# Optimization experiments

Hardware: AMD Instinct MI355X
Metric: run time of the kernel (lower is better)

Reference implementation:

```python
import jax, jax.numpy as jnp
import numpy as np

FEATURE_DIM = 1024
HIDDEN_DIM = FEATURE_DIM // 4  # MetaNet default: max(input_dim//4, output_dim) = 256
NUM_TASKS = 8
BATCH = 8192


def setup_inputs() -> dict:
    key = jax.random.key(0)
    ks = jax.random.split(key, 8)
    features = jax.random.normal(ks[0], (BATCH, FEATURE_DIM), dtype=jnp.float32)
    # meta_net: Linear(D->H) -> ReLU -> Linear(H->K). Scaled so coefficients straddle the threshold.
    W1 = jax.random.normal(ks[1], (HIDDEN_DIM, FEATURE_DIM), dtype=jnp.float32) * 0.02
    b1 = jax.random.normal(ks[2], (HIDDEN_DIM,), dtype=jnp.float32) * 0.01
    W2 = jax.random.normal(ks[3], (NUM_TASKS, HIDDEN_DIM), dtype=jnp.float32) * 0.1
    b2 = jax.random.normal(ks[4], (NUM_TASKS,), dtype=jnp.float32) * 0.05
    # per-task feature transforms, init randn * 0.01 as in the module
    task_mats = jax.random.normal(ks[5], (NUM_TASKS, FEATURE_DIM, FEATURE_DIM), dtype=jnp.float32) * 0.01
    # projection initialized to identity (nn.init.eye_)
    proj_W = jnp.eye(FEATURE_DIM, dtype=jnp.float32)
    base_threshold = jnp.array([0.05], dtype=jnp.float32)
    beta = jnp.array([1.0], dtype=jnp.float32)
    return {"features": features, "W1": W1, "b1": b1, "W2": W2, "b2": b2,
            "task_mats": task_mats, "proj_W": proj_W,
            "base_threshold": base_threshold, "beta": beta}


def reference(features, W1, b1, W2, b2, task_mats, proj_W, base_threshold, beta):
    # --- meta_net forward: coefficients [B, K] ---
    h = features @ W1.T + b1                    # [B, H]
    relu_h = jnp.maximum(h, 0.0)
    coeffs = relu_h @ W2.T + b2                 # [B, K]

    # --- gradient-based uncertainty: ||d coeff_k / d features_b||_2 ---
    # Jacobian of the 2-layer MLP: J[b,k,d] = sum_h W2[k,h] * relu'(h[b,h]) * W1[h,d]
    mask = (h > 0).astype(features.dtype)       # [B, H]
    J = jnp.einsum('kh,bh,hd->bkd', W2, mask, W1)   # [B, K, D]
    unc = jnp.sqrt(jnp.sum(J * J, axis=-1))     # [B, K]
    mx = jnp.max(unc)
    unc = jnp.where(mx > 0, unc / mx, unc)
    # torch computes this on detached features with create_graph=False -> non-differentiable
    unc = jax.lax.stop_gradient(unc)

    # --- adaptive gating ---
    base = jax.nn.softplus(base_threshold)                  # [1]
    thresholds = base * (1.0 + jax.nn.relu(beta) * unc)     # [B, K]
    gated = jnp.where(jnp.abs(coeffs) < thresholds, 0.0, coeffs)  # [B, K]

    # --- sequential weighted task-vector combination (blockwise=False) ---
    x = features                                # [B, D]
    for j in range(task_mats.shape[0]):         # small fixed K, structurally sequential
        x = x + gated[:, j:j + 1] * (x @ task_mats[j])
    return x @ proj_W.T                         # [B, D]
```

## Files before the change

### kernel.cpp

```cpp
#include <hip/hip_runtime.h>


typedef float  f32x4  __attribute__((ext_vector_type(4)));
typedef __bf16 bf16x8 __attribute__((ext_vector_type(8)));
typedef _Float16 f16x8 __attribute__((ext_vector_type(8)));
typedef _Float16 f16x4 __attribute__((ext_vector_type(4)));

__device__ __forceinline__ unsigned short f2bf(float x) {
  return __builtin_bit_cast(unsigned short, (__bf16)x);
}
__device__ __forceinline__ float bf2f(unsigned short u) {
  return (float)__builtin_bit_cast(__bf16, u);
}
__device__ __forceinline__ void ldsload16(void* lds, const void* g) {
  __builtin_amdgcn_global_load_lds(
      (const __attribute__((address_space(1))) void*)g,
      (__attribute__((address_space(3))) void*)lds, 16, 0, 0);
}


__global__ __launch_bounds__(256) void k_initsplit(const float* __restrict__ F,
                                                   _Float16* __restrict__ hi,
                                                   _Float16* __restrict__ lo,
                                                   float* __restrict__ xout,
                                                   unsigned short* __restrict__ xhA,
                                                   unsigned short* __restrict__ xhB) {
  size_t i = (size_t)blockIdx.x * 256 + threadIdx.x;
  float4 f = *(const float4*)&F[i * 4];
  _Float16 h0 = (_Float16)f.x, h1 = (_Float16)f.y, h2 = (_Float16)f.z, h3 = (_Float16)f.w;
  *(f16x4*)&hi[i * 4] = (f16x4){h0, h1, h2, h3};
  *(f16x4*)&lo[i * 4] = (f16x4){(_Float16)((f.x - (float)h0) * 2048.0f),
                                (_Float16)((f.y - (float)h1) * 2048.0f),
                                (_Float16)((f.z - (float)h2) * 2048.0f),
                                (_Float16)((f.w - (float)h3) * 2048.0f)};
  *(float4*)&xout[i * 4] = f;
  ushort4 u;
  u.x = f2bf(f.x); u.y = f2bf(f.y); u.z = f2bf(f.z); u.w = f2bf(f.w);
  *(ushort4*)&xhA[i * 4] = u;
  *(ushort4*)&xhB[i * 4] = u;
}

__global__ __launch_bounds__(256) void k_split(const float* __restrict__ src,
                                               _Float16* __restrict__ hi,
                                               _Float16* __restrict__ lo) {
  size_t i = (size_t)blockIdx.x * 256 + threadIdx.x;
  float4 f = *(const float4*)&src[i * 4];
  _Float16 h0 = (_Float16)f.x, h1 = (_Float16)f.y, h2 = (_Float16)f.z, h3 = (_Float16)f.w;
  *(f16x4*)&hi[i * 4] = (f16x4){h0, h1, h2, h3};
  *(f16x4*)&lo[i * 4] = (f16x4){(_Float16)((f.x - (float)h0) * 2048.0f),
                                (_Float16)((f.y - (float)h1) * 2048.0f),
                                (_Float16)((f.z - (float)h2) * 2048.0f),
                                (_Float16)((f.w - (float)h3) * 2048.0f)};
}

__global__ __launch_bounds__(256) void k_gram(const float* __restrict__ W1,
                                              float* __restrict__ G) {
  __shared__ float Wa[16][33], Wb[16][33];
  int t = threadIdx.x, ti = t & 15, tj = t >> 4;
  int bi = blockIdx.x, bj = blockIdx.y;
  float acc = 0.f;
  for (int kc = 0; kc < 1024; kc += 32) {
    __syncthreads();
    for (int e = t; e < 512; e += 256) {
      int r = e >> 5, k = e & 31;
      Wa[r][k] = W1[(size_t)(bi * 16 + r) * 1024 + kc + k];
      Wb[r][k] = W1[(size_t)(bj * 16 + r) * 1024 + kc + k];
    }
    __syncthreads();
#pragma unroll
    for (int k = 0; k < 32; k++) acc += Wa[ti][k] * Wb[tj][k];
  }
  G[(size_t)(bi * 16 + ti) * 256 + bj * 16 + tj] = acc;
}

__global__ __launch_bounds__(256) void k_prepA(const float* __restrict__ W2,
                                               const float* __restrict__ G,
                                               unsigned short* __restrict__ Bk,
                                               unsigned int* __restrict__ mx,
                                               int* __restrict__ cnt,
                                               int* __restrict__ cnt2,
                                               unsigned int* __restrict__ flag) {
  int k = blockIdx.x >> 8, hr = blockIdx.x & 255, t = threadIdx.x;
  if (blockIdx.x == 0) {
    if (t == 0) { *mx = 0u; *flag = 1u; }
    if (t < 8) { cnt[t] = 0; cnt2[t] = 0; }
  }
  float v = W2[k * 256 + hr] * W2[k * 256 + t] * G[(size_t)hr * 256 + t];
  float hi = bf2f(f2bf(v));
  float lo = v - hi;
  unsigned short* row = &Bk[((size_t)k * 256 + hr) * 512];
  row[t] = f2bf(hi);
  row[256 + t] = f2bf(lo);
}

__global__ __launch_bounds__(256) void k_maskcoef(const float* __restrict__ h,
                                                  const float* __restrict__ W2,
                                                  const float* __restrict__ b2,
                                                  unsigned short* __restrict__ Mb,
                                                  unsigned int* __restrict__ Mbits,
                                                  float* __restrict__ coeffs) {
  __shared__ float W2s[2048];
  __shared__ unsigned sw[4][8];
  int t = threadIdx.x;
  for (int e = t; e < 2048; e += 256) W2s[e] = W2[e];
  int w = t >> 6, l = t & 63;
  int row = blockIdx.x * 4 + w;
  float4 hv = *(const float4*)&h[(size_t)row * 256 + l * 4];
  ushort4 mv;
  mv.x = hv.x > 0.f ? 0x3F80 : 0; mv.y = hv.y > 0.f ? 0x3F80 : 0;
  mv.z = hv.z > 0.f ? 0x3F80 : 0; mv.w = hv.w > 0.f ? 0x3F80 : 0;
  *(ushort4*)&Mb[(size_t)row * 256 + l * 4] = mv;
  unsigned nib = (hv.x > 0.f ? 1u : 0u) | (hv.y > 0.f ? 2u : 0u) |
                 (hv.z > 0.f ? 4u : 0u) | (hv.w > 0.f ? 8u : 0u);
  if (l < 8) sw[w][l] = 0u;
  __syncthreads();
  atomicOr(&sw[w][l >> 3], nib << ((l & 7) * 4));
  __syncthreads();
  if (l < 8) Mbits[row * 8 + l] = sw[w][l];
  float r0 = fmaxf(hv.x, 0.f), r1 = fmaxf(hv.y, 0.f);
  float r2 = fmaxf(hv.z, 0.f), r3 = fmaxf(hv.w, 0.f);
#pragma unroll
  for (int k = 0; k < 8; k++) {
    const float* wr = &W2s[k * 256 + l * 4];
    float p = r0 * wr[0] + r1 * wr[1] + r2 * wr[2] + r3 * wr[3];
    p += __shfl_xor(p, 1);  p += __shfl_xor(p, 2);  p += __shfl_xor(p, 4);
    p += __shfl_xor(p, 8);  p += __shfl_xor(p, 16); p += __shfl_xor(p, 32);
    if (l == 0) coeffs[row * 8 + k] = p + b2[k];
  }
}

__global__ __launch_bounds__(256) void k_max(const float* __restrict__ unc2,
                                             unsigned int* __restrict__ mx) {
  int i = blockIdx.x * 256 + threadIdx.x;
  float v = 0.f;
  for (; i < 65536; i += 64 * 256) v = fmaxf(v, unc2[i]);
#pragma unroll
  for (int d = 1; d < 64; d <<= 1) v = fmaxf(v, __shfl_xor(v, d));
  __shared__ float sm[4];
  if ((threadIdx.x & 63) == 0) sm[threadIdx.x >> 6] = v;
  __syncthreads();
  if (threadIdx.x == 0) {
    v = fmaxf(fmaxf(sm[0], sm[1]), fmaxf(sm[2], sm[3]));
    atomicMax(mx, __float_as_uint(v));
  }
}

__global__ __launch_bounds__(256) void k_gateidx(const float* __restrict__ coeffs,
                                                 const float* __restrict__ unc2,
                                                 const unsigned int* __restrict__ mxb,
                                                 const float* __restrict__ btp,
                                                 const float* __restrict__ betap,
                                                 unsigned short* __restrict__ rowidx,
                                                 float* __restrict__ gcomp,
                                                 int* __restrict__ cnt,
                                                 unsigned short* __restrict__ rowidx2,
                                                 int* __restrict__ cnt2) {
  __shared__ int lc[8], base[8], lc2[8], base2[8];
  __shared__ float sgv[256];
  int t = threadIdx.x;
  if (t < 8) { lc[t] = 0; lc2[t] = 0; }
  __syncthreads();
  int i = blockIdx.x * 256 + t;
  float c = coeffs[i];
  float u2 = fmaxf(unc2[i], 0.f);
  float un = sqrtf(u2);
  float m = sqrtf(__uint_as_float(*mxb));
  float u = (m > 0.f) ? un / m : un;
  float base_t = (float)log1p(exp((double)btp[0]));
  float br = fmaxf(betap[0], 0.f);
  float thr = base_t * (1.0f + br * u);
  float gv = (fabsf(c) < thr) ? 0.f : c;
  sgv[t] = gv;
  int jj = i & 7, row = i >> 3, slot = -1;
  if (gv != 0.f) slot = atomicAdd(&lc[jj], 1);
  __syncthreads();
  int slot2 = -1;
  if (jj >= 1 && gv == 0.f && sgv[t - 1] != 0.f) slot2 = atomicAdd(&lc2[jj], 1);
  __syncthreads();
  if (t < 8) {
    base[t]  = lc[t]  ? atomicAdd(&cnt[t],  lc[t])  : 0;
    base2[t] = lc2[t] ? atomicAdd(&cnt2[t], lc2[t]) : 0;
  }
  __syncthreads();
  if (slot >= 0) {
    int pos = base[jj] + slot;
    rowidx[jj * 8192 + pos] = (unsigned short)row;
    gcomp[jj * 8192 + pos] = gv;
  }
  if (slot2 >= 0)
    rowidx2[jj * 8192 + base2[jj] + slot2] = (unsigned short)row;
}

__global__ __launch_bounds__(256) void k_prepT(const float* __restrict__ TM,
                                               unsigned short* __restrict__ Tb) {
  __shared__ float Ls[64][65];
  int bid = blockIdx.x;
  int jj = bid >> 8, kt = (bid >> 4) & 15, nt = bid & 15;
  int t = threadIdx.x;
  int r = t >> 2, c0 = (t & 3) * 16;
  const float* src = TM + (size_t)jj * 1048576 + (size_t)(kt * 64 + r) * 1024 + nt * 64 + c0;
  float4 v0 = *(const float4*)&src[0];
  float4 v1 = *(const float4*)&src[4];
  float4 v2 = *(const float4*)&src[8];
  float4 v3 = *(const float4*)&src[12];
  float tmp[16] = {v0.x, v0.y, v0.z, v0.w, v1.x, v1.y, v1.z, v1.w,
                   v2.x, v2.y, v2.z, v2.w, v3.x, v3.y, v3.z, v3.w};
#pragma unroll
  for (int i = 0; i < 16; i++) Ls[r][c0 + i] = tmp[i];
  __syncthreads();
  int nr = t >> 2, kc = (t & 3) * 16;
  union { unsigned short s[16]; uint4 v[2]; } p;
#pragma unroll
  for (int i = 0; i < 16; i++) p.s[i] = f2bf(Ls[kc + i][nr]);
  unsigned short* dst = Tb + (size_t)jj * 1048576 + (size_t)(nt * 64 + nr) * 1024 + kt * 64 + kc;
  *(uint4*)&dst[0] = p.v[0];
  *(uint4*)&dst[8] = p.v[1];
}

__global__ __launch_bounds__(256) void k_prepP2(const float* __restrict__ P,
                                                unsigned short* __restrict__ Pb,
                                                unsigned int* __restrict__ flag) {
  size_t i = (size_t)blockIdx.x * 256 + threadIdx.x;
  float4 f = *(const float4*)&P[i * 4];
  ushort4 u;
  u.x = f2bf(f.x); u.y = f2bf(f.y); u.z = f2bf(f.z); u.w = f2bf(f.w);
  *(ushort4*)&Pb[i * 4] = u;
  size_t e = i * 4;
  bool bad = false;
#pragma unroll
  for (int s = 0; s < 4; s++) {
    size_t ee = e + s;
    float exp = ((ee >> 10) == (ee & 1023)) ? 1.0f : 0.0f;
    float got = (s == 0) ? f.x : (s == 1) ? f.y : (s == 2) ? f.z : f.w;
    if (got != exp) bad = true;
  }
  if (bad) atomicAnd(flag, 0u);
}


__global__ __launch_bounds__(256) void k_gemm_h2(const _Float16* __restrict__ Fhi,
                                                 const _Float16* __restrict__ Flo,
                                                 const _Float16* __restrict__ W1h,
                                                 const _Float16* __restrict__ W1l,
                                                 const float* __restrict__ b1,
                                                 float* __restrict__ hout) {
  __shared__ __attribute__((aligned(16))) _Float16 Ah[64 * 32];
  __shared__ __attribute__((aligned(16))) _Float16 Al[64 * 32];
  __shared__ __attribute__((aligned(16))) _Float16 Bh[64 * 32];
  __shared__ __attribute__((aligned(16))) _Float16 Bl[64 * 32];
  int t = threadIdx.x, w = t >> 6, l = t & 63, q = l >> 4, li = l & 15;
  int wm = w >> 1, wn = w & 1;
  int ib = blockIdx.x, jb = blockIdx.y;
  f32x4 acc0[2][2] = {}, acc1[2][2] = {};
  int row = t >> 2, kc = (t & 3) * 8;
  for (int k0 = 0; k0 < 1024; k0 += 32) {
    __syncthreads();
    size_t ao = (size_t)(ib * 64 + row) * 1024 + k0 + kc;
    size_t bo = (size_t)(jb * 64 + row) * 1024 + k0 + kc;
    ldsload16((void*)(Ah + (w * 64) * 8), Fhi + ao);
    ldsload16((void*)(Al + (w * 64) * 8), Flo + ao);
    ldsload16((void*)(Bh + (w * 64) * 8), W1h + bo);
    ldsload16((void*)(Bl + (w * 64) * 8), W1l + bo);
    __syncthreads();
    f16x8 ah[2], al[2], bh[2], bl[2];
#pragma unroll
    for (int mt = 0; mt < 2; mt++) {
      ah[mt] = *(const f16x8*)&Ah[(wm * 32 + mt * 16 + li) * 32 + q * 8];
      al[mt] = *(const f16x8*)&Al[(wm * 32 + mt * 16 + li) * 32 + q * 8];
    }
#pragma unroll
    for (int nt = 0; nt < 2; nt++) {
      bh[nt] = *(const f16x8*)&Bh[(wn * 32 + nt * 16 + li) * 32 + q * 8];
      bl[nt] = *(const f16x8*)&Bl[(wn * 32 + nt * 16 + li) * 32 + q * 8];
    }
#pragma unroll
    for (int mt = 0; mt < 2; mt++)
#pragma unroll
      for (int nt = 0; nt < 2; nt++) {
        acc0[mt][nt] = __builtin_amdgcn_mfma_f32_16x16x32_f16(ah[mt], bh[nt], acc0[mt][nt], 0, 0, 0);
        acc1[mt][nt] = __builtin_amdgcn_mfma_f32_16x16x32_f16(ah[mt], bl[nt], acc1[mt][nt], 0, 0, 0);
        acc1[mt][nt] = __builtin_amdgcn_mfma_f32_16x16x32_f16(al[mt], bh[nt], acc1[mt][nt], 0, 0, 0);
      }
  }
  const float sc = 1.0f / 2048.0f;
#pragma unroll
  for (int mt = 0; mt < 2; mt++) {
    int grow = ib * 64 + wm * 32 + mt * 16 + q * 4;
#pragma unroll
    for (int nt = 0; nt < 2; nt++) {
      int gcol = jb * 64 + wn * 32 + nt * 16 + li;
      float bb = b1[gcol];
#pragma unroll
      for (int r = 0; r < 4; r++)
        hout[(size_t)(grow + r) * 256 + gcol] = acc0[mt][nt][r] + acc1[mt][nt][r] * sc + bb;
    }
  }
}

__global__ __launch_bounds__(256) void k_gemm_unc(const unsigned short* __restrict__ Mb,
                                                  const unsigned short* __restrict__ BkAll,
                                                  const unsigned int* __restrict__ Mbits,
                                                  float* __restrict__ unc2) {
  __shared__ __attribute__((aligned(16))) unsigned short As[64 * 32];
  __shared__ __attribute__((aligned(16))) unsigned short Bs[256 * 32];
  int t = threadIdx.x, w = t >> 6, l = t & 63, q = l >> 4, li = l & 15;
  int rb = blockIdx.x, kidx = blockIdx.y;
  const unsigned short* Bk = BkAll + (size_t)kidx * 256 * 512;
  f32x4 acc[16] = {};
  for (int k0 = 0; k0 < 512; k0 += 32) {
    __syncthreads();
    {
      int row = t >> 2, kc = (t & 3) * 8;
      int kk = (k0 & 255) + kc;
      ldsload16((void*)(As + (w * 64) * 8), Mb + (size_t)(rb * 64 + row) * 256 + kk);
    }
#pragma unroll
    for (int i = 0; i < 4; i++) {
      int idx = i * 256 + t, row = idx >> 2, kc = (idx & 3) * 8;
      ldsload16((void*)(Bs + (i * 256 + w * 64) * 8), Bk + (size_t)row * 512 + k0 + kc);
    }
    __syncthreads();
    bf16x8 av = *(const bf16x8*)&As[(w * 16 + li) * 32 + q * 8];
#pragma unroll
    for (int nt = 0; nt < 16; nt++) {
      bf16x8 bv = *(const bf16x8*)&Bs[(nt * 16 + li) * 32 + q * 8];
      acc[nt] = __builtin_amdgcn_mfma_f32_16x16x32_bf16(av, bv, acc[nt], 0, 0, 0);
    }
  }
  int row0 = rb * 64 + w * 16 + q * 4;
  unsigned mw[4][8];
#pragma unroll
  for (int r = 0; r < 4; r++) {
    const uint4* p = (const uint4*)&Mbits[(size_t)(row0 + r) * 8];
    uint4 a = p[0], b = p[1];
    mw[r][0] = a.x; mw[r][1] = a.y; mw[r][2] = a.z; mw[r][3] = a.w;
    mw[r][4] = b.x; mw[r][5] = b.y; mw[r][6] = b.z; mw[r][7] = b.w;
  }
  float ps[4] = {0.f, 0.f, 0.f, 0.f};
#pragma unroll
  for (int nt = 0; nt < 16; nt++) {
    int word = nt >> 1, sh = (nt & 1) * 16 + li;
#pragma unroll
    for (int r = 0; r < 4; r++)
      if ((mw[r][word] >> sh) & 1u) ps[r] += acc[nt][r];
  }
#pragma unroll
  for (int r = 0; r < 4; r++) {
    float v = ps[r];
    v += __shfl_xor(v, 1); v += __shfl_xor(v, 2);
    v += __shfl_xor(v, 4); v += __shfl_xor(v, 8);
    ps[r] = v;
  }
  if (li == 0)
#pragma unroll
    for (int r = 0; r < 4; r++) unc2[(size_t)(row0 + r) * 8 + kidx] = ps[r];
}

__global__ __launch_bounds__(1024) void k_chain8(const unsigned short* __restrict__ cur,
                                                 unsigned short* __restrict__ nxt,
                                                 const unsigned short* __restrict__ Tb,
                                                 const unsigned short* __restrict__ rowidx,
                                                 const int* __restrict__ cnt,
                                                 const unsigned short* __restrict__ rowidx2,
                                                 const int* __restrict__ cnt2,
                                                 const float* __restrict__ gcomp,
                                                 float* __restrict__ xout, int j) {
  int Mj = min(max(cnt[j], 0), 8192);
  __shared__ __attribute__((aligned(16))) unsigned short As[64 * 512];
  __shared__ __attribute__((aligned(16))) unsigned short Bs[64 * 512];
  int t = threadIdx.x, w = t >> 6, l = t & 63, q = l >> 4, li = l & 15;
  int wm = w >> 2, wn = w & 3;
  int bx = blockIdx.x, jb = blockIdx.y;
  int bid = jb * 16 + bx;
  const unsigned short* ridx = rowidx + j * 8192;
  {
    int M2 = min(max(cnt2[j], 0), 8192);
    for (int cm2 = bid; cm2 < M2; cm2 += 256) {
      int row = rowidx2[j * 8192 + cm2] & 8191;
      if (t < 128)
        *(uint4*)&nxt[(size_t)row * 1024 + t * 8] =
            *(const uint4*)&cur[(size_t)row * 1024 + t * 8];
    }
  }
  for (int ib = bx; ib * 64 < Mj; ib += 16) {
    f32x4 acc = {};
#pragma unroll 1
    for (int half = 0; half < 2; half++) {
      __syncthreads();
#pragma unroll
      for (int i = 0; i < 4; i++) {
        int slot = i * 1024 + t;
        int r = slot >> 6, kcs = slot & 63;
        int kcg = kcs ^ (r & 7);
        int cm = ib * 64 + r;
        int grow = ridx[cm < Mj ? cm : Mj - 1] & 8191;
        ldsload16((void*)(As + (size_t)(i * 1024 + w * 64) * 8),
                  cur + (size_t)grow * 1024 + half * 512 + kcg * 8);
      }
#pragma unroll
      for (int i = 0; i < 4; i++) {
        int slot = i * 1024 + t;
        int n = slot >> 6, kcs = slot & 63;
        int kcg = kcs ^ (n & 7);
        ldsload16((void*)(Bs + (size_t)(i * 1024 + w * 64) * 8),
                  Tb + (size_t)(jb * 64 + n) * 1024 + half * 512 + kcg * 8);
      }
      __syncthreads();
#pragma unroll
      for (int s = 0; s < 16; s++) {
        int r = wm * 16 + li;
        bf16x8 av = *(const bf16x8*)&As[((size_t)r * 64 + ((s * 4 + q) ^ (r & 7))) * 8];
        int n = wn * 16 + li;
        bf16x8 bv = *(const bf16x8*)&Bs[((size_t)n * 64 + ((s * 4 + q) ^ (n & 7))) * 8];
        acc = __builtin_amdgcn_mfma_f32_16x16x32_bf16(av, bv, acc, 0, 0, 0);
      }
    }
#pragma unroll
    for (int r = 0; r < 4; r++) {
      int cm = ib * 64 + wm * 16 + q * 4 + r;
      if (cm >= Mj) continue;
      int grow = ridx[cm] & 8191;
      float g = gcomp[j * 8192 + cm];
      size_t off = (size_t)grow * 1024 + jb * 64 + wn * 16 + li;
      float xv = fmaf(g, acc[r], xout[off]);
      xout[off] = xv;
      nxt[off] = f2bf(xv);
    }
  }
}

__global__ __launch_bounds__(256) void k_proj3(const unsigned short* __restrict__ xcur,
                                               const unsigned short* __restrict__ Pb,
                                               float* __restrict__ out,
                                               const unsigned int* __restrict__ flag) {
  if (*flag) return;
  __shared__ __attribute__((aligned(16))) unsigned short As[128 * 32];
  __shared__ __attribute__((aligned(16))) unsigned short Bs[128 * 32];
  int t = threadIdx.x, w = t >> 6, l = t & 63, q = l >> 4, li = l & 15;
  int wm = w >> 1, wn = w & 1;
  int ib = blockIdx.x, jb = blockIdx.y;
  f32x4 acc[4][4] = {};
  for (int k0 = 0; k0 < 1024; k0 += 32) {
    __syncthreads();
    const unsigned short* ga = xcur + (size_t)(ib * 128) * 1024 + k0;
    const unsigned short* gb = Pb + (size_t)(jb * 128) * 1024 + k0;
#pragma unroll
    for (int i = 0; i < 2; i++) {
      int idx = i * 256 + t, row = idx >> 2, kc = (idx & 3) * 8;
      ldsload16((void*)(As + (i * 256 + w * 64) * 8), ga + (size_t)row * 1024 + kc);
      ldsload16((void*)(Bs + (i * 256 + w * 64) * 8), gb + (size_t)row * 1024 + kc);
    }
    __syncthreads();
    bf16x8 av[4], bv[4];
#pragma unroll
    for (int mt = 0; mt < 4; mt++)
      av[mt] = *(const bf16x8*)&As[(wm * 64 + mt * 16 + li) * 32 + q * 8];
#pragma unroll
    for (int nt = 0; nt < 4; nt++)
      bv[nt] = *(const bf16x8*)&Bs[(wn * 64 + nt * 16 + li) * 32 + q * 8];
#pragma unroll
    for (int mt = 0; mt < 4; mt++)
#pragma unroll
      for (int nt = 0; nt < 4; nt++)
        acc[mt][nt] = __builtin_amdgcn_mfma_f32_16x16x32_bf16(av[mt], bv[nt], acc[mt][nt], 0, 0, 0);
  }
#pragma unroll
  for (int mt = 0; mt < 4; mt++) {
    int grow = ib * 128 + wm * 64 + mt * 16 + q * 4;
#pragma unroll
    for (int nt = 0; nt < 4; nt++) {
      int gcol = jb * 128 + wn * 64 + nt * 16 + li;
#pragma unroll
      for (int r = 0; r < 4; r++)
        out[(size_t)(grow + r) * 1024 + gcol] = acc[mt][nt][r];
    }
  }
}


extern "C" void kernel_launch(void* const* d_in, const int* in_sizes, int n_in,
                              void* d_out, int out_size, void* d_ws, size_t ws_size,
                              hipStream_t stream) {
  const float* F    = (const float*)d_in[0];
  const float* W1   = (const float*)d_in[1];
  const float* b1   = (const float*)d_in[2];
  const float* W2   = (const float*)d_in[3];
  const float* b2   = (const float*)d_in[4];
  const float* TM   = (const float*)d_in[5];
  const float* PW   = (const float*)d_in[6];
  const float* bt   = (const float*)d_in[7];
  const float* beta = (const float*)d_in[8];

  char* w = (char*)d_ws;
  float*          hbuf   = (float*)         (w + 0);
  unsigned short* Mb     = (unsigned short*)(w + 8388608);
  unsigned int*   Mbits  = (unsigned int*)  (w + 12582912);
  float*          coeffs = (float*)         (w + 12845056);
  float*          unc2   = (float*)         (w + 13107200);
  float*          G      = (float*)         (w + 13369344);
  unsigned short* Bk     = (unsigned short*)(w + 13631488);
  _Float16*       W1h    = (_Float16*)      (w + 15728640);
  _Float16*       W1l    = (_Float16*)      (w + 16252928);
  unsigned short* Tb     = (unsigned short*)(w + 0);
  char*           buf0   =                  (w + 16777216);
  char*           buf1   =                  (w + 33554432);
  unsigned int*   mx     = (unsigned int*)  (w + 50331648);
  int*            cnt    = (int*)           (w + 50331652);
  int*            cnt2   = (int*)           (w + 50331684);
  unsigned int*   flag   = (unsigned int*)  (w + 50331716);
  unsigned short* rowidx = (unsigned short*)(w + 50332160);
  unsigned short* rowidx2= (unsigned short*)(w + 50463232);
  float*          gcomp  = (float*)         (w + 50594304);
  unsigned short* xhA    = (unsigned short*)(w + 50856448);
  unsigned short* xhB    = (unsigned short*)(w + 67633664);
  float* xout = (float*)d_out;

  k_initsplit<<<8192, 256, 0, stream>>>(F, (_Float16*)buf0, (_Float16*)buf1, xout, xhA, xhB);
  k_split<<<256, 256, 0, stream>>>(W1, W1h, W1l);
  k_gram<<<dim3(16, 16), 256, 0, stream>>>(W1, G);
  k_gemm_h2<<<dim3(128, 4), 256, 0, stream>>>((const _Float16*)buf0, (const _Float16*)buf1,
                                              W1h, W1l, b1, hbuf);
  k_maskcoef<<<2048, 256, 0, stream>>>(hbuf, W2, b2, Mb, Mbits, coeffs);
  k_prepA<<<2048, 256, 0, stream>>>(W2, G, Bk, mx, cnt, cnt2, flag);
  k_gemm_unc<<<dim3(128, 8), 256, 0, stream>>>(Mb, Bk, Mbits, unc2);
  k_max<<<64, 256, 0, stream>>>(unc2, mx);
  k_gateidx<<<256, 256, 0, stream>>>(coeffs, unc2, mx, bt, beta,
                                     rowidx, gcomp, cnt, rowidx2, cnt2);

  k_prepT<<<2048, 256, 0, stream>>>(TM, Tb);
  for (int j = 0; j < 8; j++) {
    const unsigned short* cur = (j & 1) ? xhB : xhA;
    unsigned short*       nxt = (j & 1) ? xhA : xhB;
    k_chain8<<<dim3(16, 16), 1024, 0, stream>>>(cur, nxt, Tb + (size_t)j * 1048576,
                                                rowidx, cnt, rowidx2, cnt2,
                                                gcomp, xout, j);
  }

  unsigned short* Pb = (unsigned short*)buf1;
  k_prepP2<<<1024, 256, 0, stream>>>(PW, Pb, flag);
  k_proj3<<<dim3(64, 8), 256, 0, stream>>>(xhA, Pb, xout, flag);
}
```

Before: 362.3 us.

## Swizzle LDS tiles and retile uncertainty GEMM to 128x256 with 2D warps

Adds an XOR-style rotation swizzle to the LDS layout in the h GEMM and the uncertainty GEMM, so fragment reads avoid bank conflicts. The uncertainty GEMM now runs 512 threads per block on 128-row tiles. Warps are laid out in a 4x4 grid of MFMA tiles, which gives more A/B reuse per load, and the masked reduction goes through a shared-memory cross-warp sum. The cost is fewer blocks and more LDS per block.

```diff
diff --git a/kernel.cpp b/kernel.cpp
--- a/kernel.cpp
+++ b/kernel.cpp
@@ -252,11 +252,11 @@
   int wm = w >> 1, wn = w & 1;
   int ib = blockIdx.x, jb = blockIdx.y;
   f32x4 acc0[2][2] = {}, acc1[2][2] = {};
-  int row = t >> 2, kc = (t & 3) * 8;
+  int srow = t >> 2, sg = (((t & 3) - (srow >> 1)) & 3) * 8;
   for (int k0 = 0; k0 < 1024; k0 += 32) {
     __syncthreads();
-    size_t ao = (size_t)(ib * 64 + row) * 1024 + k0 + kc;
-    size_t bo = (size_t)(jb * 64 + row) * 1024 + k0 + kc;
+    size_t ao = (size_t)(ib * 64 + srow) * 1024 + k0 + sg;
+    size_t bo = (size_t)(jb * 64 + srow) * 1024 + k0 + sg;
     ldsload16((void*)(Ah + (w * 64) * 8), Fhi + ao);
     ldsload16((void*)(Al + (w * 64) * 8), Flo + ao);
     ldsload16((void*)(Bh + (w * 64) * 8), W1h + bo);
@@ -265,13 +265,17 @@
     f16x8 ah[2], al[2], bh[2], bl[2];
 #pragma unroll
     for (int mt = 0; mt < 2; mt++) {
-      ah[mt] = *(const f16x8*)&Ah[(wm * 32 + mt * 16 + li) * 32 + q * 8];
-      al[mt] = *(const f16x8*)&Al[(wm * 32 + mt * 16 + li) * 32 + q * 8];
+      int r = wm * 32 + mt * 16 + li;
+      int c = ((q + (r >> 1)) & 3) * 8;
+      ah[mt] = *(const f16x8*)&Ah[r * 32 + c];
+      al[mt] = *(const f16x8*)&Al[r * 32 + c];
     }
 #pragma unroll
     for (int nt = 0; nt < 2; nt++) {
-      bh[nt] = *(const f16x8*)&Bh[(wn * 32 + nt * 16 + li) * 32 + q * 8];
-      bl[nt] = *(const f16x8*)&Bl[(wn * 32 + nt * 16 + li) * 32 + q * 8];
+      int rr = wn * 32 + nt * 16 + li;
+      int c = ((q + (rr >> 1)) & 3) * 8;
+      bh[nt] = *(const f16x8*)&Bh[rr * 32 + c];
+      bl[nt] = *(const f16x8*)&Bl[rr * 32 + c];
     }
 #pragma unroll
     for (int mt = 0; mt < 2; mt++)
@@ -297,63 +301,73 @@
   }
 }
 
-__global__ __launch_bounds__(256) void k_gemm_unc(const unsigned short* __restrict__ Mb,
-                                                  const unsigned short* __restrict__ BkAll,
-                                                  const unsigned int* __restrict__ Mbits,
-                                                  float* __restrict__ unc2) {
-  __shared__ __attribute__((aligned(16))) unsigned short As[64 * 32];
+__global__ __launch_bounds__(512) void k_gemm_unc2(const unsigned short* __restrict__ Mb,
+                                                   const unsigned short* __restrict__ BkAll,
+                                                   const unsigned int* __restrict__ Mbits,
+                                                   float* __restrict__ unc2) {
+  __shared__ __attribute__((aligned(16))) unsigned short As[128 * 32];
   __shared__ __attribute__((aligned(16))) unsigned short Bs[256 * 32];
+  __shared__ float Red[128][4];
   int t = threadIdx.x, w = t >> 6, l = t & 63, q = l >> 4, li = l & 15;
+  int wm = w >> 2, wn = w & 3;
   int rb = blockIdx.x, kidx = blockIdx.y;
   const unsigned short* Bk = BkAll + (size_t)kidx * 256 * 512;
-  f32x4 acc[16] = {};
+  f32x4 acc[4][4] = {};
   for (int k0 = 0; k0 < 512; k0 += 32) {
     __syncthreads();
     {
-      int row = t >> 2, kc = (t & 3) * 8;
-      int kk = (k0 & 255) + kc;
-      ldsload16((void*)(As + (w * 64) * 8), Mb + (size_t)(rb * 64 + row) * 256 + kk);
-    }
-#pragma unroll
-    for (int i = 0; i < 4; i++) {
-      int idx = i * 256 + t, row = idx >> 2, kc = (idx & 3) * 8;
-      ldsload16((void*)(Bs + (i * 256 + w * 64) * 8), Bk + (size_t)row * 512 + k0 + kc);
-    }
-    __syncthreads();
-    bf16x8 av = *(const bf16x8*)&As[(w * 16 + li) * 32 + q * 8];
-#pragma unroll
-    for (int nt = 0; nt < 16; nt++) {
-      bf16x8 bv = *(const bf16x8*)&Bs[(nt * 16 + li) * 32 + q * 8];
-      acc[nt] = __builtin_amdgcn_mfma_f32_16x16x32_bf16(av, bv, acc[nt], 0, 0, 0);
-    }
-  }
-  int row0 = rb * 64 + w * 16 + q * 4;
-  unsigned mw[4][8];
-#pragma unroll
-  for (int r = 0; r < 4; r++) {
-    const uint4* p = (const uint4*)&Mbits[(size_t)(row0 + r) * 8];
-    uint4 a = p[0], b = p[1];
-    mw[r][0] = a.x; mw[r][1] = a.y; mw[r][2] = a.z; mw[r][3] = a.w;
-    mw[r][4] = b.x; mw[r][5] = b.y; mw[r][6] = b.z; mw[r][7] = b.w;
-  }
-  float ps[4] = {0.f, 0.f, 0.f, 0.f};
-#pragma unroll
-  for (int nt = 0; nt < 16; nt++) {
-    int word = nt >> 1, sh = (nt & 1) * 16 + li;
-#pragma unroll
-    for (int r = 0; r < 4; r++)
-      if ((mw[r][word] >> sh) & 1u) ps[r] += acc[nt][r];
-  }
-#pragma unroll
-  for (int r = 0; r < 4; r++) {
-    float v = ps[r];
-    v += __shfl_xor(v, 1); v += __shfl_xor(v, 2);
-    v += __shfl_xor(v, 4); v += __shfl_xor(v, 8);
-    ps[r] = v;
-  }
-  if (li == 0)
-#pragma unroll
-    for (int r = 0; r < 4; r++) unc2[(size_t)(row0 + r) * 8 + kidx] = ps[r];
+      int row = t >> 2, g = (((t & 3) - (row >> 1)) & 3) * 8;
+      ldsload16((void*)(As + (size_t)(w * 64) * 8),
+                Mb + (size_t)(rb * 128 + row) * 256 + (k0 & 255) + g);
+    }
+#pragma unroll
+    for (int i = 0; i < 2; i++) {
+      int idx = i * 512 + t, row = idx >> 2, g = (((idx & 3) - (row >> 1)) & 3) * 8;
+      ldsload16((void*)(Bs + (size_t)(i * 512 + w * 64) * 8),
+                Bk + (size_t)row * 512 + k0 + g);
+    }
+    __syncthreads();
+    bf16x8 av[4], bv[4];
+#pragma unroll
+    for (int mt = 0; mt < 4; mt++) {
+      int r = wm * 64 + mt * 16 + li;
+      av[mt] = *(const bf16x8*)&As[r * 32 + ((q + (r >> 1)) & 3) * 8];
+    }
+#pragma unroll
+    for (int nt = 0; nt < 4; nt++) {
+      int rc = wn * 64 + nt * 16 + li;
+      bv[nt] = *(const bf16x8*)&Bs[rc * 32 + ((q + (rc >> 1)) & 3) * 8];
+    }
+#pragma unroll
+    for (int mt = 0; mt < 4; mt++)
+#pragma unroll
+      for (int nt = 0; nt < 4; nt++)
+        acc[mt][nt] = __builtin_amdgcn_mfma_f32_16x16x32_bf16(av[mt], bv[nt], acc[mt][nt], 0, 0, 0);
+  }
+#pragma unroll
+  for (int mt = 0; mt < 4; mt++) {
+#pragma unroll
+    for (int r = 0; r < 4; r++) {
+      int rl = wm * 64 + mt * 16 + q * 4 + r;
+      int grow = rb * 128 + rl;
+      unsigned m0 = Mbits[(size_t)grow * 8 + wn * 2];
+      unsigned m1 = Mbits[(size_t)grow * 8 + wn * 2 + 1];
+      float p = 0.f;
+#pragma unroll
+      for (int nt = 0; nt < 4; nt++) {
+        unsigned mword = (nt < 2) ? m0 : m1;
+        int sh = (nt & 1) * 16 + li;
+        if ((mword >> sh) & 1u) p += acc[mt][nt][r];
+      }
+      p += __shfl_xor(p, 1); p += __shfl_xor(p, 2);
+      p += __shfl_xor(p, 4); p += __shfl_xor(p, 8);
+      if (li == 0) Red[rl][wn] = p;
+    }
+  }
+  __syncthreads();
+  if (t < 128)
+    unc2[(size_t)(rb * 128 + t) * 8 + kidx] =
+        Red[t][0] + Red[t][1] + Red[t][2] + Red[t][3];
 }
 
 __global__ __launch_bounds__(1024) void k_chain8(const unsigned short* __restrict__ cur,
@@ -522,7 +536,7 @@
                                               W1h, W1l, b1, hbuf);
   k_maskcoef<<<2048, 256, 0, stream>>>(hbuf, W2, b2, Mb, Mbits, coeffs);
   k_prepA<<<2048, 256, 0, stream>>>(W2, G, Bk, mx, cnt, cnt2, flag);
-  k_gemm_unc<<<dim3(128, 8), 256, 0, stream>>>(Mb, Bk, Mbits, unc2);
+  k_gemm_unc2<<<dim3(64, 8), 512, 0, stream>>>(Mb, Bk, Mbits, unc2);
   k_max<<<64, 256, 0, stream>>>(unc2, mx);
   k_gateidx<<<256, 256, 0, stream>>>(coeffs, unc2, mx, bt, beta,
                                      rowidx, gcomp, cnt, rowidx2, cnt2);
```

Measured after the change: 352.8 us. -2.6%, faster.
